# Optimization experiments

Measured on AMD Instinct MI355X. Metric: run time of the kernel, lower is better.

Reference implementation:

```python
import math
import jax, jax.numpy as jnp
import numpy as np

V, D, H, F, L = 32128, 768, 12, 3072, 12
NUM_BUCKETS, MAX_DIST = 32, 128
B, S = 16, 512
EPS = 1e-6


def _rel_bucket(rel_pos, num_buckets=NUM_BUCKETS, max_distance=MAX_DIST):
    # bidirectional T5 bucketing
    num_buckets //= 2
    ret = (rel_pos > 0).astype(jnp.int32) * num_buckets
    n = jnp.abs(rel_pos)
    max_exact = num_buckets // 2
    is_small = n < max_exact
    large = max_exact + (
        jnp.log(n.astype(jnp.float32) / max_exact)
        / math.log(max_distance / max_exact)
        * (num_buckets - max_exact)
    ).astype(jnp.int32)
    large = jnp.minimum(large, num_buckets - 1)
    return ret + jnp.where(is_small, n.astype(jnp.int32), large)


def t5_layernorm(x, w):
    # RMS norm: no mean subtraction, no bias
    var = jnp.mean(x * x, axis=-1, keepdims=True)
    return x * jax.lax.rsqrt(var + EPS) * w


def setup_inputs() -> dict:
    key = jax.random.key(0)
    ks = jax.random.split(key, 12)
    sc = 0.02
    inp = {
        "tokens": jax.random.randint(ks[0], (B, S), 0, V, dtype=jnp.int64),
        "emb": jax.random.normal(ks[1], (V, D), jnp.float32) * sc,
        "rel_bias": jax.random.normal(ks[2], (NUM_BUCKETS, H), jnp.float32) * sc,
        "ln1_w": jnp.ones((L, D), jnp.float32),
        "wq": jax.random.normal(ks[3], (L, D, D), jnp.float32) * sc,
        "wk": jax.random.normal(ks[4], (L, D, D), jnp.float32) * sc,
        "wv": jax.random.normal(ks[5], (L, D, D), jnp.float32) * sc,
        "wo": jax.random.normal(ks[6], (L, D, D), jnp.float32) * sc,
        "ln2_w": jnp.ones((L, D), jnp.float32),
        "w1": jax.random.normal(ks[7], (L, D, F), jnp.float32) * sc,
        "w2": jax.random.normal(ks[8], (L, F, D), jnp.float32) * sc,
        "ln_final_w": jnp.ones((D,), jnp.float32),
    }
    return inp


def _attn(x, pos_bias, wq, wk, wv, wo):
    b, s, d = x.shape
    dh = d // H
    q = (x @ wq).reshape(b, s, H, dh).transpose(0, 2, 1, 3)
    k = (x @ wk).reshape(b, s, H, dh).transpose(0, 2, 1, 3)
    v = (x @ wv).reshape(b, s, H, dh).transpose(0, 2, 1, 3)
    # T5: NO 1/sqrt(dh) scaling; add bucketed relative-position bias
    scores = jnp.einsum("bhqd,bhkd->bhqk", q, k) + pos_bias[None]  # [B,H,S,S]
    a = jax.nn.softmax(scores, axis=-1)
    o = jnp.einsum("bhqk,bhkd->bhqd", a, v)
    o = o.transpose(0, 2, 1, 3).reshape(b, s, d)
    return o @ wo


def reference(tokens, emb, rel_bias, ln1_w, wq, wk, wv, wo, ln2_w, w1, w2, ln_final_w):
    x = emb[tokens]  # [B,S,D]
    s = tokens.shape[1]
    pos = jnp.arange(s)
    buckets = _rel_bucket(pos[None, :] - pos[:, None])  # [S,S]
    pos_bias = rel_bias[buckets].transpose(2, 0, 1)  # [H,S,S], computed once (layer 0)
    for i in range(L):
        h = t5_layernorm(x, ln1_w[i])
        x = x + _attn(h, pos_bias, wq[i], wk[i], wv[i], wo[i])
        h = t5_layernorm(x, ln2_w[i])
        x = x + jax.nn.relu(h @ w1[i]) @ w2[i]
    return t5_layernorm(x, ln_final_w)
```

## Files before the change

### kernel.cpp

```cpp
#include <hip/hip_runtime.h>
#include <hip/hip_bf16.h>

typedef unsigned short u16;
typedef unsigned int   u32;
typedef __attribute__((ext_vector_type(8))) __bf16 bf16x8;
typedef __attribute__((ext_vector_type(4))) float  f32x4;
typedef __attribute__((ext_vector_type(4))) u16    u16x4;
typedef __attribute__((ext_vector_type(4))) u32    u32x4;

#define SEQ     512
#define DMODEL  768
#define NHEAD   12
#define DHEAD   64
#define FDIM    3072
#define NLAYER  12
#define NROWS   8192
#define QKVN    2304

__device__ __forceinline__ u16 f2bf(float f) {
  union { float f; u32 u; } x; x.f = f;
  u32 r = x.u + 0x7fffu + ((x.u >> 16) & 1u);
  return (u16)(r >> 16);
}
__device__ __forceinline__ float u2f(u32 u) { union { u32 u; float f; } x; x.u = u; return x.f; }

__global__ __launch_bounds__(256) void k_transpose_cvt(const float* __restrict__ in,
                                                       u16* __restrict__ out, int K, int N,
                                                       size_t istride, size_t ostride) {
  __shared__ float tile[32][33];
  in  += (size_t)blockIdx.z * istride;
  out += (size_t)blockIdx.z * ostride;
  int nb = blockIdx.x * 32, kb = blockIdx.y * 32;
  int tx = threadIdx.x, ty = threadIdx.y;
#pragma unroll
  for (int i = 0; i < 4; i++)
    tile[ty + 8 * i][tx] = in[(size_t)(kb + ty + 8 * i) * N + nb + tx];
  __syncthreads();
#pragma unroll
  for (int i = 0; i < 4; i++)
    out[(size_t)(nb + ty + 8 * i) * K + kb + tx] = f2bf(tile[tx][ty + 8 * i]);
}

__global__ __launch_bounds__(256) void k_embed(const int* __restrict__ tokens,
                                               const float* __restrict__ emb,
                                               float* __restrict__ x) {
  int idx = blockIdx.x * 256 + threadIdx.x;
  int row = idx / 192, c4 = idx % 192;
  int tok = tokens[row];
  reinterpret_cast<float4*>(x + (size_t)row * DMODEL)[c4] =
      reinterpret_cast<const float4*>(emb + (size_t)tok * DMODEL)[c4];
}

__global__ __launch_bounds__(256) void k_biaslut(const float* __restrict__ rel_bias,
                                                 float* __restrict__ lut) {
  int idx = blockIdx.x * 256 + threadIdx.x;
  int h = idx >> 10, i = idx & 1023;
  int rel = i - 511;
  int ret = rel > 0 ? 16 : 0;
  int n = rel < 0 ? -rel : rel;
  int b;
  if (n < 8) {
    b = n;
  } else {
    float r = logf((float)n * 0.125f) / 2.772588722239781f * 8.0f;
    int lg = 8 + (int)r;
    b = lg < 15 ? lg : 15;
  }
  b += ret;
  lut[idx] = rel_bias[b * NHEAD + h];
}

template <int BF16OUT>
__global__ __launch_bounds__(256) void k_rmsnorm(const float* __restrict__ x,
                                                 const float* __restrict__ w,
                                                 void* __restrict__ out) {
  int row = blockIdx.x * 4 + (threadIdx.x >> 6);
  int lane = threadIdx.x & 63;
  const float4* xr = reinterpret_cast<const float4*>(x + (size_t)row * DMODEL);
  float4 a = xr[lane], b = xr[lane + 64], c = xr[lane + 128];
  float ss = a.x * a.x + a.y * a.y + a.z * a.z + a.w * a.w
           + b.x * b.x + b.y * b.y + b.z * b.z + b.w * b.w
           + c.x * c.x + c.y * c.y + c.z * c.z + c.w * c.w;
#pragma unroll
  for (int off = 1; off < 64; off <<= 1) ss += __shfl_xor(ss, off);
  float sc = rsqrtf(ss * (1.0f / 768.0f) + 1e-6f);
  const float4* wr = reinterpret_cast<const float4*>(w);
  float4 w0 = wr[lane], w1 = wr[lane + 64], w2 = wr[lane + 128];
  if (BF16OUT) {
    u16x4* o = reinterpret_cast<u16x4*>((u16*)out + (size_t)row * DMODEL);
    u16x4 v0, v1, v2;
    v0[0] = f2bf(a.x * sc * w0.x); v0[1] = f2bf(a.y * sc * w0.y);
    v0[2] = f2bf(a.z * sc * w0.z); v0[3] = f2bf(a.w * sc * w0.w);
    v1[0] = f2bf(b.x * sc * w1.x); v1[1] = f2bf(b.y * sc * w1.y);
    v1[2] = f2bf(b.z * sc * w1.z); v1[3] = f2bf(b.w * sc * w1.w);
    v2[0] = f2bf(c.x * sc * w2.x); v2[1] = f2bf(c.y * sc * w2.y);
    v2[2] = f2bf(c.z * sc * w2.z); v2[3] = f2bf(c.w * sc * w2.w);
    o[lane] = v0; o[lane + 64] = v1; o[lane + 128] = v2;
  } else {
    float4* o = reinterpret_cast<float4*>((float*)out + (size_t)row * DMODEL);
    float4 v0, v1, v2;
    v0.x = a.x * sc * w0.x; v0.y = a.y * sc * w0.y; v0.z = a.z * sc * w0.z; v0.w = a.w * sc * w0.w;
    v1.x = b.x * sc * w1.x; v1.y = b.y * sc * w1.y; v1.z = b.z * sc * w1.z; v1.w = b.w * sc * w1.w;
    v2.x = c.x * sc * w2.x; v2.y = c.y * sc * w2.y; v2.z = c.z * sc * w2.z; v2.w = c.w * sc * w2.w;
    o[lane] = v0; o[lane + 64] = v1; o[lane + 128] = v2;
  }
}

__device__ __forceinline__ void gload_lds16(const void* g, void* l) {
  __builtin_amdgcn_global_load_lds((const __attribute__((address_space(1))) void*)g,
                                   (__attribute__((address_space(3))) void*)l, 16, 0, 0);
}

template <int EPI>
__global__ __launch_bounds__(512, 2) void k_gemm(const u16* __restrict__ A, const u16* __restrict__ Bt,
                                                 u16* __restrict__ outb, float* __restrict__ outf,
                                                 int M, int N, int K) {
  __shared__ u16 lds[3 * 24576];
  const int NT = K >> 6;
  int tid = threadIdx.x;
  int lane = tid & 63, wid = tid >> 6;
  int lr = lane & 15, lh = lane >> 4;
  int wm = wid >> 1, wn = wid & 1;

  int gx = gridDim.x;
  int gm = gridDim.y;
  int nwg = gx * gm;
  int linear = blockIdx.y * gx + blockIdx.x;
  int cpx = nwg >> 3;
  int swz = (linear & 7) * cpx + (linear >> 3);
  int bm = (swz % gm) * 256;
  int bn = (swz / gm) * 128;

  const u16* Ab = A  + (size_t)bm * K;
  const u16* Bb = Bt + (size_t)bn * K;

  int cswz = (((tid & 3) ^ ((tid >> 2) & 3) ^ ((tid >> 4) & 3))) * 8;
  int arow = tid >> 2;

  f32x4 acc[4][4] = {};

  auto STAGE_A = [&](int kt, u16* dst) {
#pragma unroll
    for (int a = 0; a < 4; a++) {
      const u16* src = Ab + (size_t)((a & 1) * 128 + arow) * K + kt * 64 + (a >> 1) * 32 + cswz;
      gload_lds16(src, dst + a * 4096 + (size_t)tid * 8);
    }
  };
  auto STAGE_B = [&](int kt, u16* dst) {
#pragma unroll
    for (int b = 0; b < 2; b++) {
      const u16* src = Bb + (size_t)arow * K + kt * 64 + b * 32 + cswz;
      gload_lds16(src, dst + 16384 + b * 4096 + (size_t)tid * 8);
    }
  };

  STAGE_A(0, lds);
  STAGE_B(0, lds);
  STAGE_A(1, lds + 24576);
  STAGE_B(1, lds + 24576);
  asm volatile("s_waitcnt vmcnt(6)" ::: "memory");
  __builtin_amdgcn_s_barrier();

  bf16x8 af[4], bfr[4];
  int rsw = ((lr & 3) ^ ((lr >> 2) & 3)) * 8;
  int chunk = (lh * 8) ^ rsw;

#define DSA(KK)                                                                 \
  _Pragma("unroll") for (int i = 0; i < 4; i++) {                               \
    int row = wm * 64 + i * 16 + lr;                                            \
    af[i] = *reinterpret_cast<const bf16x8*>(cur + (KK) * 8192 + row * 32 + chunk); \
  }
#define DSB(KK)                                                                 \
  _Pragma("unroll") for (int n = 0; n < 4; n++) {                               \
    int row = wn * 64 + n * 16 + lr;                                            \
    bfr[n] = *reinterpret_cast<const bf16x8*>(cur + 16384 + (KK) * 4096 + row * 32 + chunk); \
  }
#define MFMA16                                                                  \
  __builtin_amdgcn_s_setprio(1);                                                \
  _Pragma("unroll") for (int i = 0; i < 4; i++)                                 \
  _Pragma("unroll") for (int n = 0; n < 4; n++)                                 \
    acc[i][n] = __builtin_amdgcn_mfma_f32_16x16x32_bf16(af[i], bfr[n], acc[i][n], 0, 0, 0); \
  __builtin_amdgcn_s_setprio(0);
#define BAR_LGKM                                                                \
  __builtin_amdgcn_s_barrier();                                                 \
  asm volatile("s_waitcnt lgkmcnt(0)" ::: "memory");                            \
  __builtin_amdgcn_sched_barrier(0);

  int cur_s = 0;
  for (int t = 0; t < NT; ++t) {
    const u16* cur = lds + cur_s * 24576;
    int dst_s = cur_s + 2; if (dst_s >= 3) dst_s -= 3;
    u16* dst = lds + dst_s * 24576;
    int t2 = (t + 2 < NT) ? t + 2 : t + 2 - NT;

    DSA(0)
    DSB(0)
    STAGE_A(t2, dst);
    BAR_LGKM
    MFMA16
    __builtin_amdgcn_s_barrier();

    DSA(1)
    DSB(1)
    STAGE_B(t2, dst);
    BAR_LGKM
    MFMA16
    asm volatile("s_waitcnt vmcnt(6)" ::: "memory");
    __builtin_amdgcn_s_barrier();

    cur_s += 1; if (cur_s >= 3) cur_s -= 3;
  }
#undef DSA
#undef DSB
#undef MFMA16
#undef BAR_LGKM

#pragma unroll
  for (int i = 0; i < 4; i++)
#pragma unroll
    for (int n = 0; n < 4; n++)
#pragma unroll
      for (int r = 0; r < 4; r++) {
        int row = bm + wm * 64 + i * 16 + lh * 4 + r;
        int col = bn + wn * 64 + n * 16 + lr;
        size_t idx = (size_t)row * N + col;
        float v = acc[i][n][r];
        if (EPI == 0)      outb[idx] = f2bf(v);
        else if (EPI == 1) outb[idx] = f2bf(v > 0.f ? v : 0.f);
        else               outf[idx] += v;
      }
}

__global__ __launch_bounds__(256) void k_vtrans(const u16* __restrict__ qkv, u16* __restrict__ vt) {
  __shared__ u16 t[32][33];
  int bh = blockIdx.z;
  int b = bh / NHEAD, h = bh % NHEAD;
  int d0 = blockIdx.x * 32, s0 = blockIdx.y * 32;
  int tx = threadIdx.x, ty = threadIdx.y;
  const u16* src = qkv + (size_t)(b * SEQ + s0) * QKVN + 2 * DMODEL + h * DHEAD + d0;
#pragma unroll
  for (int i = 0; i < 4; i++)
    t[ty + 8 * i][tx] = src[(size_t)(ty + 8 * i) * QKVN + tx];
  __syncthreads();
  u16* dst = vt + ((size_t)bh * DHEAD + d0) * SEQ + s0;
#pragma unroll
  for (int i = 0; i < 4; i++)
    dst[(size_t)(ty + 8 * i) * SEQ + tx] = t[tx][ty + 8 * i];
}

__global__ __launch_bounds__(256) void k_attn(const u16* __restrict__ qkv,
                                              const u16* __restrict__ vt,
                                              const float* __restrict__ lutg,
                                              u16* __restrict__ ob) {
  __shared__ __align__(16) float lut[1024];
  __shared__ __align__(16) u16 Ks[2][4096];
  __shared__ __align__(16) u16 Vs[2][4096];
  __shared__ __align__(16) u16 Ps[4][2048];
  int b = blockIdx.x / NHEAD, h = blockIdx.x % NHEAD;
  int qt = blockIdx.y;
  int tid = threadIdx.x;
  int lane = tid & 63, wid = tid >> 6;
  int lr = lane & 15, lh = lane >> 4;
  int q0 = qt * 128 + wid * 32;

  reinterpret_cast<float4*>(lut)[tid] = reinterpret_cast<const float4*>(lutg + h * 1024)[tid];

  bf16x8 aq[2][2];
#pragma unroll
  for (int m = 0; m < 2; m++) {
    const u16* qp = qkv + (size_t)(b * SEQ + q0 + m * 16 + lr) * QKVN + h * DHEAD;
#pragma unroll
    for (int kk = 0; kk < 2; kk++)
      aq[m][kk] = *reinterpret_cast<const bf16x8*>(qp + kk * 32 + lh * 8);
  }

  float mrun[2][4], lpart[2][4];
  f32x4 acc_o[2][4] = {};
#pragma unroll
  for (int m = 0; m < 2; m++)
#pragma unroll
    for (int r = 0; r < 4; r++) { mrun[m][r] = -3.0e38f; lpart[m][r] = 0.f; }

  int srow = tid >> 3, sc8 = tid & 7;
  int scs = (sc8 ^ (srow & 7)) << 3;
  const u16* kbase = qkv + (size_t)(b * SEQ + srow) * QKVN + DMODEL + h * DHEAD + scs;
  const u16* vbase = vt + ((size_t)blockIdx.x * DHEAD + srow) * SEQ + scs;

  auto STAGE = [&](int kt, int bufi) {
    int kv0 = kt << 6;
    gload_lds16(kbase + (size_t)kv0 * QKVN,        &Ks[bufi][tid * 8]);
    gload_lds16(kbase + (size_t)(kv0 + 32) * QKVN, &Ks[bufi][2048 + tid * 8]);
    gload_lds16(vbase + kv0,                       &Vs[bufi][tid * 8]);
    gload_lds16(vbase + 32 * SEQ + kv0,            &Vs[bufi][2048 + tid * 8]);
  };

  STAGE(0, 0);
  asm volatile("s_waitcnt vmcnt(0) lgkmcnt(0)" ::: "memory");
  __builtin_amdgcn_s_barrier();

  int ibase = 511 + lr - q0 - lh * 4;
  u16* pw = Ps[wid];

  for (int kt = 0; kt < 8; kt++) {
    int cb = kt & 1;
    __builtin_amdgcn_s_barrier();
    STAGE((kt + 1) & 7, cb ^ 1);
    asm volatile("s_waitcnt vmcnt(4)" ::: "memory");
    __builtin_amdgcn_s_barrier();

    const u16* KsC = Ks[cb];
    const u16* VsC = Vs[cb];
    int kv0 = kt << 6;

    f32x4 sc[2][4] = {};
#pragma unroll
    for (int kk = 0; kk < 2; kk++) {
      bf16x8 bk[4];
#pragma unroll
      for (int n = 0; n < 4; n++) {
        int row = n * 16 + lr;
        int c = (kk * 4 + lh) ^ (lr & 7);
        bk[n] = *reinterpret_cast<const bf16x8*>(KsC + row * 64 + c * 8);
      }
#pragma unroll
      for (int m = 0; m < 2; m++)
#pragma unroll
        for (int n = 0; n < 4; n++)
          sc[m][n] = __builtin_amdgcn_mfma_f32_16x16x32_bf16(aq[m][kk], bk[n], sc[m][n], 0, 0, 0);
    }

    int pred = 1;
    float vmax[2][4];
#pragma unroll
    for (int m = 0; m < 2; m++)
#pragma unroll
      for (int r = 0; r < 4; r++) {
        int ib = ibase + kv0 - m * 16 - r;
#pragma unroll
        for (int n = 0; n < 4; n++)
          sc[m][n][r] += lut[ib + n * 16];
        float v = fmaxf(fmaxf(sc[m][0][r], sc[m][1][r]), fmaxf(sc[m][2][r], sc[m][3][r]));
        v = fmaxf(v, __shfl_xor(v, 1));
        v = fmaxf(v, __shfl_xor(v, 2));
        v = fmaxf(v, __shfl_xor(v, 4));
        v = fmaxf(v, __shfl_xor(v, 8));
        vmax[m][r] = v;
        pred = pred && (v <= mrun[m][r] + 8.0f);
      }
    if (!__all(pred)) {
#pragma unroll
      for (int m = 0; m < 2; m++)
#pragma unroll
        for (int r = 0; r < 4; r++) {
          float mo = mrun[m][r];
          float mn = fmaxf(mo, vmax[m][r]);
          float corr = __expf(mo - mn);
          mrun[m][r] = mn;
          lpart[m][r] *= corr;
#pragma unroll
          for (int n = 0; n < 4; n++) acc_o[m][n][r] *= corr;
        }
    }
#pragma unroll
    for (int m = 0; m < 2; m++)
#pragma unroll
      for (int r = 0; r < 4; r++) {
        float mm = mrun[m][r];
        int prow = m * 16 + lh * 4 + r;
        int pbse = prow * 64;
        int sw = prow & 7;
        float lp = lpart[m][r];
#pragma unroll
        for (int n = 0; n < 4; n++) {
          float pv = __expf(sc[m][n][r] - mm);
          lp += pv;
          pw[pbse + ((((n << 1) | (lr >> 3)) ^ sw) << 3) + (lr & 7)] = f2bf(pv);
        }
        lpart[m][r] = lp;
      }

    asm volatile("s_waitcnt lgkmcnt(0)" ::: "memory");
    __builtin_amdgcn_sched_barrier(0);
#pragma unroll
    for (int kk = 0; kk < 2; kk++) {
      bf16x8 bvv[4], ap[2];
#pragma unroll
      for (int n = 0; n < 4; n++) {
        int row = n * 16 + lr;
        int c = (kk * 4 + lh) ^ (lr & 7);
        bvv[n] = *reinterpret_cast<const bf16x8*>(VsC + row * 64 + c * 8);
      }
#pragma unroll
      for (int m = 0; m < 2; m++) {
        int row = m * 16 + lr;
        int c = (kk * 4 + lh) ^ (lr & 7);
        ap[m] = *reinterpret_cast<const bf16x8*>(pw + row * 64 + c * 8);
      }
#pragma unroll
      for (int m = 0; m < 2; m++)
#pragma unroll
        for (int n = 0; n < 4; n++)
          acc_o[m][n] = __builtin_amdgcn_mfma_f32_16x16x32_bf16(ap[m], bvv[n], acc_o[m][n], 0, 0, 0);
    }
  }

#pragma unroll
  for (int m = 0; m < 2; m++)
#pragma unroll
    for (int r = 0; r < 4; r++) {
      float l = lpart[m][r];
      l += __shfl_xor(l, 1);
      l += __shfl_xor(l, 2);
      l += __shfl_xor(l, 4);
      l += __shfl_xor(l, 8);
      float inv = 1.f / l;
      size_t orow = (size_t)(b * SEQ + q0 + m * 16 + lh * 4 + r);
#pragma unroll
      for (int n = 0; n < 4; n++)
        ob[orow * DMODEL + h * DHEAD + n * 16 + lr] = f2bf(acc_o[m][n][r] * inv);
    }
}

extern "C" void kernel_launch(void* const* d_in, const int* in_sizes, int n_in,
                              void* d_out, int out_size, void* d_ws, size_t ws_size,
                              hipStream_t stream) {
  const int*   tokens = (const int*)  d_in[0];
  const float* emb    = (const float*)d_in[1];
  const float* relb   = (const float*)d_in[2];
  const float* ln1w   = (const float*)d_in[3];
  const float* wq     = (const float*)d_in[4];
  const float* wk     = (const float*)d_in[5];
  const float* wv     = (const float*)d_in[6];
  const float* wo     = (const float*)d_in[7];
  const float* ln2w   = (const float*)d_in[8];
  const float* w1     = (const float*)d_in[9];
  const float* w2     = (const float*)d_in[10];
  const float* lnfw   = (const float*)d_in[11];
  float* out = (float*)d_out;

  char* p = (char*)d_ws;
  auto carve = [&](size_t bytes) { char* r = p; p += (bytes + 255) & ~(size_t)255; return r; };
  const size_t DD = (size_t)DMODEL * DMODEL, DF = (size_t)DMODEL * FDIM;

  u16*   wqkv_t = (u16*)carve(NLAYER * 3 * DD * 2);
  u16*   wo_t   = (u16*)carve(NLAYER * DD * 2);
  u16*   w1_t   = (u16*)carve(NLAYER * DF * 2);
  u16*   w2_t   = (u16*)carve(NLAYER * DF * 2);
  float* x      = (float*)carve((size_t)NROWS * DMODEL * 4);
  u16*   hbuf   = (u16*)carve((size_t)NROWS * DMODEL * 2);
  u16*   qkvbuf = (u16*)carve((size_t)NROWS * QKVN * 2);
  u16*   abuf   = (u16*)carve((size_t)NROWS * DMODEL * 2);
  u16*   fbuf   = (u16*)carve((size_t)NROWS * FDIM * 2);
  float* lutbuf = (float*)carve((size_t)NHEAD * 1024 * 4);
  u16*   vtbuf  = fbuf;

  dim3 tb(32, 8);
  k_transpose_cvt<<<dim3(24, 24, NLAYER), tb, 0, stream>>>(wq, wqkv_t,          DMODEL, DMODEL, DD, 3 * DD);
  k_transpose_cvt<<<dim3(24, 24, NLAYER), tb, 0, stream>>>(wk, wqkv_t + DD,     DMODEL, DMODEL, DD, 3 * DD);
  k_transpose_cvt<<<dim3(24, 24, NLAYER), tb, 0, stream>>>(wv, wqkv_t + 2 * DD, DMODEL, DMODEL, DD, 3 * DD);
  k_transpose_cvt<<<dim3(24, 24, NLAYER), tb, 0, stream>>>(wo, wo_t,            DMODEL, DMODEL, DD, DD);
  k_transpose_cvt<<<dim3(96, 24, NLAYER), tb, 0, stream>>>(w1, w1_t,            DMODEL, FDIM,   DF, DF);
  k_transpose_cvt<<<dim3(24, 96, NLAYER), tb, 0, stream>>>(w2, w2_t,            FDIM, DMODEL,   DF, DF);

  k_embed<<<NROWS * 192 / 256, 256, 0, stream>>>(tokens, emb, x);
  k_biaslut<<<48, 256, 0, stream>>>(relb, lutbuf);

  for (int i = 0; i < NLAYER; i++) {
    k_rmsnorm<1><<<NROWS / 4, 256, 0, stream>>>(x, ln1w + i * DMODEL, hbuf);
    k_gemm<0><<<dim3(18, 32), 512, 0, stream>>>(hbuf, wqkv_t + (size_t)i * 3 * DD, qkvbuf, nullptr, NROWS, QKVN, DMODEL);
    k_vtrans<<<dim3(2, 16, 192), tb, 0, stream>>>(qkvbuf, vtbuf);
    k_attn<<<dim3(192, 4), 256, 0, stream>>>(qkvbuf, vtbuf, lutbuf, abuf);
    k_gemm<2><<<dim3(6, 32),  512, 0, stream>>>(abuf, wo_t + (size_t)i * DD, nullptr, x, NROWS, DMODEL, DMODEL);
    k_rmsnorm<1><<<NROWS / 4, 256, 0, stream>>>(x, ln2w + i * DMODEL, hbuf);
    k_gemm<1><<<dim3(24, 32), 512, 0, stream>>>(hbuf, w1_t + (size_t)i * DF, fbuf, nullptr, NROWS, FDIM, DMODEL);
    k_gemm<2><<<dim3(6, 32),  512, 0, stream>>>(fbuf, w2_t + (size_t)i * DF, nullptr, x, NROWS, DMODEL, FDIM);
  }
  k_rmsnorm<0><<<NROWS / 4, 256, 0, stream>>>(x, lnfw, out);
}
```

Measured before the change: 3.602 ms.

## Retile GEMM to 128x192 blocks with 4 waves and 32-wide K steps

Reworks the GEMM kernel from 256x128 tiles with 8 waves and K-step 64 to 128x192 tiles with 4 waves and K-step 32. Each wave now owns a 128x48 output slice, reuses its B fragments across both M halves, and the LDS footprint per stage shrinks. Grids change so the projection and FFN GEMMs launch more, smaller blocks, which should improve fill for the N=768 GEMMs (4x64=256 blocks instead of 6x32=192). The trade-offs are twice as many barriers per K, fewer waves to hide latency, and lower arithmetic intensity per block.

After: 3.731 ms. 3.6% more time.

```diff
diff --git a/kernel.cpp b/kernel.cpp
--- a/kernel.cpp
+++ b/kernel.cpp
@@ -112,15 +112,14 @@
 }
 
 template <int EPI>
-__global__ __launch_bounds__(512, 2) void k_gemm(const u16* __restrict__ A, const u16* __restrict__ Bt,
+__global__ __launch_bounds__(256, 2) void k_gemm(const u16* __restrict__ A, const u16* __restrict__ Bt,
                                                  u16* __restrict__ outb, float* __restrict__ outf,
                                                  int M, int N, int K) {
-  __shared__ u16 lds[3 * 24576];
-  const int NT = K >> 6;
+  __shared__ u16 lds[3 * 10240];
+  const int NT = K >> 5;
   int tid = threadIdx.x;
   int lane = tid & 63, wid = tid >> 6;
   int lr = lane & 15, lh = lane >> 4;
-  int wm = wid >> 1, wn = wid & 1;
 
   int gx = gridDim.x;
   int gm = gridDim.y;
@@ -128,58 +127,60 @@
   int linear = blockIdx.y * gx + blockIdx.x;
   int cpx = nwg >> 3;
   int swz = (linear & 7) * cpx + (linear >> 3);
-  int bm = (swz % gm) * 256;
-  int bn = (swz / gm) * 128;
+  int bm = (swz % gm) * 128;
+  int bn = (swz / gm) * 192;
 
   const u16* Ab = A  + (size_t)bm * K;
   const u16* Bb = Bt + (size_t)bn * K;
 
-  int cswz = (((tid & 3) ^ ((tid >> 2) & 3) ^ ((tid >> 4) & 3))) * 8;
-  int arow = tid >> 2;
-
-  f32x4 acc[4][4] = {};
+  f32x4 acc[8][3] = {};
 
   auto STAGE_A = [&](int kt, u16* dst) {
 #pragma unroll
-    for (int a = 0; a < 4; a++) {
-      const u16* src = Ab + (size_t)((a & 1) * 128 + arow) * K + kt * 64 + (a >> 1) * 32 + cswz;
-      gload_lds16(src, dst + a * 4096 + (size_t)tid * 8);
+    for (int a = 0; a < 2; a++) {
+      int elem = a * 256 + tid;
+      int row = elem >> 2, ch = elem & 3;
+      int chs = ch ^ (row & 3) ^ ((row >> 2) & 3);
+      gload_lds16(Ab + (size_t)row * K + kt * 32 + chs * 8, dst + elem * 8);
     }
   };
   auto STAGE_B = [&](int kt, u16* dst) {
 #pragma unroll
-    for (int b = 0; b < 2; b++) {
-      const u16* src = Bb + (size_t)arow * K + kt * 64 + b * 32 + cswz;
-      gload_lds16(src, dst + 16384 + b * 4096 + (size_t)tid * 8);
+    for (int b = 0; b < 3; b++) {
+      int elem = b * 256 + tid;
+      int row = elem >> 2, ch = elem & 3;
+      int chs = ch ^ (row & 3) ^ ((row >> 2) & 3);
+      gload_lds16(Bb + (size_t)row * K + kt * 32 + chs * 8, dst + 4096 + elem * 8);
     }
   };
 
   STAGE_A(0, lds);
   STAGE_B(0, lds);
-  STAGE_A(1, lds + 24576);
-  STAGE_B(1, lds + 24576);
-  asm volatile("s_waitcnt vmcnt(6)" ::: "memory");
+  STAGE_A(1, lds + 10240);
+  STAGE_B(1, lds + 10240);
+  asm volatile("s_waitcnt vmcnt(5)" ::: "memory");
   __builtin_amdgcn_s_barrier();
 
-  bf16x8 af[4], bfr[4];
-  int rsw = ((lr & 3) ^ ((lr >> 2) & 3)) * 8;
-  int chunk = (lh * 8) ^ rsw;
-
-#define DSA(KK)                                                                 \
+  bf16x8 af[4], bfr[3];
+  int fsw = (lr & 3) ^ ((lr >> 2) & 3);
+  int chunk = (lh ^ fsw) * 8;
+
+#define DSA(H)                                                                  \
   _Pragma("unroll") for (int i = 0; i < 4; i++) {                               \
-    int row = wm * 64 + i * 16 + lr;                                            \
-    af[i] = *reinterpret_cast<const bf16x8*>(cur + (KK) * 8192 + row * 32 + chunk); \
-  }
-#define DSB(KK)                                                                 \
-  _Pragma("unroll") for (int n = 0; n < 4; n++) {                               \
-    int row = wn * 64 + n * 16 + lr;                                            \
-    bfr[n] = *reinterpret_cast<const bf16x8*>(cur + 16384 + (KK) * 4096 + row * 32 + chunk); \
-  }
-#define MFMA16                                                                  \
+    int row = (H) * 64 + i * 16 + lr;                                           \
+    af[i] = *reinterpret_cast<const bf16x8*>(cur + row * 32 + chunk);           \
+  }
+#define DSB                                                                     \
+  _Pragma("unroll") for (int n = 0; n < 3; n++) {                               \
+    int row = wid * 48 + n * 16 + lr;                                           \
+    bfr[n] = *reinterpret_cast<const bf16x8*>(cur + 4096 + row * 32 + chunk);   \
+  }
+#define MFMA12(H)                                                               \
   __builtin_amdgcn_s_setprio(1);                                                \
   _Pragma("unroll") for (int i = 0; i < 4; i++)                                 \
-  _Pragma("unroll") for (int n = 0; n < 4; n++)                                 \
-    acc[i][n] = __builtin_amdgcn_mfma_f32_16x16x32_bf16(af[i], bfr[n], acc[i][n], 0, 0, 0); \
+  _Pragma("unroll") for (int n = 0; n < 3; n++)                                 \
+    acc[(H) * 4 + i][n] =                                                       \
+        __builtin_amdgcn_mfma_f32_16x16x32_bf16(af[i], bfr[n], acc[(H) * 4 + i][n], 0, 0, 0); \
   __builtin_amdgcn_s_setprio(0);
 #define BAR_LGKM                                                                \
   __builtin_amdgcn_s_barrier();                                                 \
@@ -188,43 +189,42 @@
 
   int cur_s = 0;
   for (int t = 0; t < NT; ++t) {
-    const u16* cur = lds + cur_s * 24576;
+    const u16* cur = lds + cur_s * 10240;
     int dst_s = cur_s + 2; if (dst_s >= 3) dst_s -= 3;
-    u16* dst = lds + dst_s * 24576;
-    int t2 = (t + 2 < NT) ? t + 2 : t + 2 - NT;
-
+    u16* dst = lds + dst_s * 10240;
+    int t2 = t + 2; if (t2 >= NT) t2 -= NT;
+
+    DSB
     DSA(0)
-    DSB(0)
     STAGE_A(t2, dst);
     BAR_LGKM
-    MFMA16
+    MFMA12(0)
     __builtin_amdgcn_s_barrier();
 
     DSA(1)
-    DSB(1)
     STAGE_B(t2, dst);
     BAR_LGKM
-    MFMA16
-    asm volatile("s_waitcnt vmcnt(6)" ::: "memory");
+    MFMA12(1)
+    asm volatile("s_waitcnt vmcnt(5)" ::: "memory");
     __builtin_amdgcn_s_barrier();
 
     cur_s += 1; if (cur_s >= 3) cur_s -= 3;
   }
 #undef DSA
 #undef DSB
-#undef MFMA16
+#undef MFMA12
 #undef BAR_LGKM
 
 #pragma unroll
-  for (int i = 0; i < 4; i++)
-#pragma unroll
-    for (int n = 0; n < 4; n++)
+  for (int mq = 0; mq < 8; mq++)
+#pragma unroll
+    for (int n = 0; n < 3; n++)
 #pragma unroll
       for (int r = 0; r < 4; r++) {
-        int row = bm + wm * 64 + i * 16 + lh * 4 + r;
-        int col = bn + wn * 64 + n * 16 + lr;
+        int row = bm + mq * 16 + lh * 4 + r;
+        int col = bn + wid * 48 + n * 16 + lr;
         size_t idx = (size_t)row * N + col;
-        float v = acc[i][n][r];
+        float v = acc[mq][n][r];
         if (EPI == 0)      outb[idx] = f2bf(v);
         else if (EPI == 1) outb[idx] = f2bf(v > 0.f ? v : 0.f);
         else               outf[idx] += v;
@@ -467,13 +467,13 @@
 
   for (int i = 0; i < NLAYER; i++) {
     k_rmsnorm<1><<<NROWS / 4, 256, 0, stream>>>(x, ln1w + i * DMODEL, hbuf);
-    k_gemm<0><<<dim3(18, 32), 512, 0, stream>>>(hbuf, wqkv_t + (size_t)i * 3 * DD, qkvbuf, nullptr, NROWS, QKVN, DMODEL);
+    k_gemm<0><<<dim3(12, 64), 256, 0, stream>>>(hbuf, wqkv_t + (size_t)i * 3 * DD, qkvbuf, nullptr, NROWS, QKVN, DMODEL);
     k_vtrans<<<dim3(2, 16, 192), tb, 0, stream>>>(qkvbuf, vtbuf);
     k_attn<<<dim3(192, 4), 256, 0, stream>>>(qkvbuf, vtbuf, lutbuf, abuf);
-    k_gemm<2><<<dim3(6, 32),  512, 0, stream>>>(abuf, wo_t + (size_t)i * DD, nullptr, x, NROWS, DMODEL, DMODEL);
+    k_gemm<2><<<dim3(4, 64),  256, 0, stream>>>(abuf, wo_t + (size_t)i * DD, nullptr, x, NROWS, DMODEL, DMODEL);
     k_rmsnorm<1><<<NROWS / 4, 256, 0, stream>>>(x, ln2w + i * DMODEL, hbuf);
-    k_gemm<1><<<dim3(24, 32), 512, 0, stream>>>(hbuf, w1_t + (size_t)i * DF, fbuf, nullptr, NROWS, FDIM, DMODEL);
-    k_gemm<2><<<dim3(6, 32),  512, 0, stream>>>(fbuf, w2_t + (size_t)i * DF, nullptr, x, NROWS, DMODEL, FDIM);
+    k_gemm<1><<<dim3(16, 64), 256, 0, stream>>>(hbuf, w1_t + (size_t)i * DF, fbuf, nullptr, NROWS, FDIM, DMODEL);
+    k_gemm<2><<<dim3(4, 64),  256, 0, stream>>>(fbuf, w2_t + (size_t)i * DF, nullptr, x, NROWS, DMODEL, FDIM);
   }
   k_rmsnorm<0><<<NROWS / 4, 256, 0, stream>>>(x, lnfw, out);
 }
```

## Use 256x256 GEMM tiles with split-K atomics for the residual projections

Applied to the files above, without the earlier changes.

The GEMM kernel moves from a 256x128 tile with a triple-buffered LDS ring to a 256x256 tile. It uses a double-buffered 64KB LDS layout with an XOR-swizzled row layout and 8 waves arranged 2x4, each computing 128x64. The A and B stages are staggered across quarter-steps. The N=768 output projection and FFN-down GEMMs now split K across grid z (2 and 4 ways) and accumulate into the fp32 residual with atomicAdd. This raises arithmetic intensity per tile and restores enough workgroups for the narrow GEMMs. The cost is atomic traffic, a nondeterministic summation order, and higher register pressure from 32 accumulators per lane.

Result: slower. 4.149 ms (+15.2%).

```diff
diff --git a/kernel.cpp b/kernel.cpp
--- a/kernel.cpp
+++ b/kernel.cpp
@@ -6,7 +6,6 @@
 typedef __attribute__((ext_vector_type(8))) __bf16 bf16x8;
 typedef __attribute__((ext_vector_type(4))) float  f32x4;
 typedef __attribute__((ext_vector_type(4))) u16    u16x4;
-typedef __attribute__((ext_vector_type(4))) u32    u32x4;
 
 #define SEQ     512
 #define DMODEL  768
@@ -22,7 +21,6 @@
   u32 r = x.u + 0x7fffu + ((x.u >> 16) & 1u);
   return (u16)(r >> 16);
 }
-__device__ __forceinline__ float u2f(u32 u) { union { u32 u; float f; } x; x.u = u; return x.f; }
 
 __global__ __launch_bounds__(256) void k_transpose_cvt(const float* __restrict__ in,
                                                        u16* __restrict__ out, int K, int N,
@@ -111,123 +109,126 @@
                                    (__attribute__((address_space(3))) void*)l, 16, 0, 0);
 }
 
+__device__ __forceinline__ bf16x8 rdfrag(const u16* base, int r, int kk, int lh) {
+  return *reinterpret_cast<const bf16x8*>(base + r * 64 + (((kk * 4 + lh) ^ (r & 7)) * 8));
+}
+
 template <int EPI>
 __global__ __launch_bounds__(512, 2) void k_gemm(const u16* __restrict__ A, const u16* __restrict__ Bt,
                                                  u16* __restrict__ outb, float* __restrict__ outf,
-                                                 int M, int N, int K) {
-  __shared__ u16 lds[3 * 24576];
-  const int NT = K >> 6;
+                                                 int M, int N, int K, int Ksub) {
+  __shared__ u16 lds[65536];
+  const int NT = Ksub >> 6;
   int tid = threadIdx.x;
   int lane = tid & 63, wid = tid >> 6;
   int lr = lane & 15, lh = lane >> 4;
-  int wm = wid >> 1, wn = wid & 1;
-
-  int gx = gridDim.x;
-  int gm = gridDim.y;
-  int nwg = gx * gm;
-  int linear = blockIdx.y * gx + blockIdx.x;
+  int wm = wid >> 2, wn = wid & 3;
+
+  int gx = gridDim.x, gm = gridDim.y;
+  int nwg = gx * gm * gridDim.z;
+  int linear = (blockIdx.z * gm + blockIdx.y) * gx + blockIdx.x;
   int cpx = nwg >> 3;
   int swz = (linear & 7) * cpx + (linear >> 3);
-  int bm = (swz % gm) * 256;
-  int bn = (swz / gm) * 128;
-
-  const u16* Ab = A  + (size_t)bm * K;
-  const u16* Bb = Bt + (size_t)bn * K;
-
-  int cswz = (((tid & 3) ^ ((tid >> 2) & 3) ^ ((tid >> 4) & 3))) * 8;
-  int arow = tid >> 2;
-
-  f32x4 acc[4][4] = {};
-
-  auto STAGE_A = [&](int kt, u16* dst) {
-#pragma unroll
-    for (int a = 0; a < 4; a++) {
-      const u16* src = Ab + (size_t)((a & 1) * 128 + arow) * K + kt * 64 + (a >> 1) * 32 + cswz;
-      gload_lds16(src, dst + a * 4096 + (size_t)tid * 8);
+  int bmi = swz % gm, rest = swz / gm;
+  int bni = rest % gx, zi = rest / gx;
+  int bm = bmi * 256, bn = bni * 256;
+  const u16* Ab = A  + (size_t)bm * K + zi * Ksub;
+  const u16* Bb = Bt + (size_t)bn * K + zi * Ksub;
+
+  f32x4 acc[8][4] = {};
+
+  auto STAGE = [&](const u16* mat, int half, int kt, int bufi, int regidx) {
+    u16* dst = lds + bufi * 32768 + regidx * 8192;
+#pragma unroll
+    for (int i = 0; i < 2; i++) {
+      int elem = i * 512 + tid;
+      int row = elem >> 3, ch = elem & 7;
+      int chs = ch ^ (row & 7);
+      gload_lds16(mat + (size_t)(half * 128 + row) * K + kt * 64 + chs * 8, dst + elem * 8);
     }
   };
-  auto STAGE_B = [&](int kt, u16* dst) {
-#pragma unroll
-    for (int b = 0; b < 2; b++) {
-      const u16* src = Bb + (size_t)arow * K + kt * 64 + b * 32 + cswz;
-      gload_lds16(src, dst + 16384 + b * 4096 + (size_t)tid * 8);
-    }
-  };
-
-  STAGE_A(0, lds);
-  STAGE_B(0, lds);
-  STAGE_A(1, lds + 24576);
-  STAGE_B(1, lds + 24576);
-  asm volatile("s_waitcnt vmcnt(6)" ::: "memory");
+
+  STAGE(Ab, 0, 0, 0, 0); STAGE(Ab, 1, 0, 0, 1);
+  STAGE(Bb, 0, 0, 0, 2); STAGE(Bb, 1, 0, 0, 3);
+  STAGE(Bb, 0, 1, 1, 2); STAGE(Bb, 1, 1, 1, 3);
+  asm volatile("s_waitcnt vmcnt(4)" ::: "memory");
   __builtin_amdgcn_s_barrier();
 
-  bf16x8 af[4], bfr[4];
-  int rsw = ((lr & 3) ^ ((lr >> 2) & 3)) * 8;
-  int chunk = (lh * 8) ^ rsw;
-
-#define DSA(KK)                                                                 \
-  _Pragma("unroll") for (int i = 0; i < 4; i++) {                               \
-    int row = wm * 64 + i * 16 + lr;                                            \
-    af[i] = *reinterpret_cast<const bf16x8*>(cur + (KK) * 8192 + row * 32 + chunk); \
-  }
-#define DSB(KK)                                                                 \
-  _Pragma("unroll") for (int n = 0; n < 4; n++) {                               \
-    int row = wn * 64 + n * 16 + lr;                                            \
-    bfr[n] = *reinterpret_cast<const bf16x8*>(cur + 16384 + (KK) * 4096 + row * 32 + chunk); \
-  }
-#define MFMA16                                                                  \
+  int bcol = (wn & 1) * 64;
+
+#define LGKM0 asm volatile("s_waitcnt lgkmcnt(0)" ::: "memory"); __builtin_amdgcn_sched_barrier(0)
+#define MFMA_Q(MQ, KK)                                                          \
   __builtin_amdgcn_s_setprio(1);                                                \
   _Pragma("unroll") for (int i = 0; i < 4; i++)                                 \
   _Pragma("unroll") for (int n = 0; n < 4; n++)                                 \
-    acc[i][n] = __builtin_amdgcn_mfma_f32_16x16x32_bf16(af[i], bfr[n], acc[i][n], 0, 0, 0); \
+    acc[(MQ) * 4 + i][n] =                                                      \
+        __builtin_amdgcn_mfma_f32_16x16x32_bf16(af[i], bfr[KK][n], acc[(MQ) * 4 + i][n], 0, 0, 0); \
   __builtin_amdgcn_s_setprio(0);
-#define BAR_LGKM                                                                \
-  __builtin_amdgcn_s_barrier();                                                 \
-  asm volatile("s_waitcnt lgkmcnt(0)" ::: "memory");                            \
-  __builtin_amdgcn_sched_barrier(0);
-
-  int cur_s = 0;
+
   for (int t = 0; t < NT; ++t) {
-    const u16* cur = lds + cur_s * 24576;
-    int dst_s = cur_s + 2; if (dst_s >= 3) dst_s -= 3;
-    u16* dst = lds + dst_s * 24576;
+    const u16* bufc = lds + (t & 1) * 32768;
+    const u16* curA = bufc + wm * 8192;
+    const u16* curB = bufc + 16384 + (wn >> 1) * 8192;
+    int t1 = (t + 1 < NT) ? t + 1 : 0;
     int t2 = (t + 2 < NT) ? t + 2 : t + 2 - NT;
-
-    DSA(0)
-    DSB(0)
-    STAGE_A(t2, dst);
-    BAR_LGKM
-    MFMA16
-    __builtin_amdgcn_s_barrier();
-
-    DSA(1)
-    DSB(1)
-    STAGE_B(t2, dst);
-    BAR_LGKM
-    MFMA16
-    asm volatile("s_waitcnt vmcnt(6)" ::: "memory");
-    __builtin_amdgcn_s_barrier();
-
-    cur_s += 1; if (cur_s >= 3) cur_s -= 3;
-  }
-#undef DSA
-#undef DSB
-#undef MFMA16
-#undef BAR_LGKM
-
-#pragma unroll
-  for (int i = 0; i < 4; i++)
-#pragma unroll
-    for (int n = 0; n < 4; n++)
+    int b1 = (t + 1) & 1, b2 = t & 1;
+    bf16x8 bfr[2][4], af[4];
+
+#pragma unroll
+    for (int n = 0; n < 4; n++) {
+      int c = bcol + n * 16 + lr;
+      bfr[0][n] = rdfrag(curB, c, 0, lh);
+      bfr[1][n] = rdfrag(curB, c, 1, lh);
+    }
+#pragma unroll
+    for (int i = 0; i < 4; i++) af[i] = rdfrag(curA, i * 16 + lr, 0, lh);
+    STAGE(Ab, 0, t1, b1, 0);
+    __builtin_amdgcn_s_barrier();
+    LGKM0;
+    MFMA_Q(0, 0)
+    __builtin_amdgcn_s_barrier();
+
+#pragma unroll
+    for (int i = 0; i < 4; i++) af[i] = rdfrag(curA, i * 16 + lr, 1, lh);
+    STAGE(Ab, 1, t1, b1, 1);
+    __builtin_amdgcn_s_barrier();
+    LGKM0;
+    MFMA_Q(0, 1)
+    __builtin_amdgcn_s_barrier();
+
+#pragma unroll
+    for (int i = 0; i < 4; i++) af[i] = rdfrag(curA, 64 + i * 16 + lr, 0, lh);
+    STAGE(Bb, 0, t2, b2, 2);
+    __builtin_amdgcn_s_barrier();
+    LGKM0;
+    MFMA_Q(1, 0)
+    __builtin_amdgcn_s_barrier();
+
+#pragma unroll
+    for (int i = 0; i < 4; i++) af[i] = rdfrag(curA, 64 + i * 16 + lr, 1, lh);
+    STAGE(Bb, 1, t2, b2, 3);
+    asm volatile("s_waitcnt vmcnt(4)" ::: "memory");
+    __builtin_amdgcn_s_barrier();
+    LGKM0;
+    MFMA_Q(1, 1)
+    __builtin_amdgcn_s_barrier();
+  }
+#undef MFMA_Q
+#undef LGKM0
+
+#pragma unroll
+  for (int mf = 0; mf < 8; mf++)
+#pragma unroll
+    for (int nf = 0; nf < 4; nf++)
 #pragma unroll
       for (int r = 0; r < 4; r++) {
-        int row = bm + wm * 64 + i * 16 + lh * 4 + r;
-        int col = bn + wn * 64 + n * 16 + lr;
+        int row = bm + wm * 128 + mf * 16 + lh * 4 + r;
+        int col = bn + wn * 64 + nf * 16 + lr;
         size_t idx = (size_t)row * N + col;
-        float v = acc[i][n][r];
+        float v = acc[mf][nf][r];
         if (EPI == 0)      outb[idx] = f2bf(v);
         else if (EPI == 1) outb[idx] = f2bf(v > 0.f ? v : 0.f);
-        else               outf[idx] += v;
+        else               atomicAdd(&outf[idx], v);
       }
 }
 
@@ -467,13 +468,17 @@
 
   for (int i = 0; i < NLAYER; i++) {
     k_rmsnorm<1><<<NROWS / 4, 256, 0, stream>>>(x, ln1w + i * DMODEL, hbuf);
-    k_gemm<0><<<dim3(18, 32), 512, 0, stream>>>(hbuf, wqkv_t + (size_t)i * 3 * DD, qkvbuf, nullptr, NROWS, QKVN, DMODEL);
+    k_gemm<0><<<dim3(9, 32, 1), 512, 0, stream>>>(hbuf, wqkv_t + (size_t)i * 3 * DD, qkvbuf, nullptr,
+                                                  NROWS, QKVN, DMODEL, DMODEL);
     k_vtrans<<<dim3(2, 16, 192), tb, 0, stream>>>(qkvbuf, vtbuf);
     k_attn<<<dim3(192, 4), 256, 0, stream>>>(qkvbuf, vtbuf, lutbuf, abuf);
-    k_gemm<2><<<dim3(6, 32),  512, 0, stream>>>(abuf, wo_t + (size_t)i * DD, nullptr, x, NROWS, DMODEL, DMODEL);
+    k_gemm<3><<<dim3(3, 32, 2), 512, 0, stream>>>(abuf, wo_t + (size_t)i * DD, nullptr, x,
+                                                  NROWS, DMODEL, DMODEL, DMODEL / 2);
     k_rmsnorm<1><<<NROWS / 4, 256, 0, stream>>>(x, ln2w + i * DMODEL, hbuf);
-    k_gemm<1><<<dim3(24, 32), 512, 0, stream>>>(hbuf, w1_t + (size_t)i * DF, fbuf, nullptr, NROWS, FDIM, DMODEL);
-    k_gemm<2><<<dim3(6, 32),  512, 0, stream>>>(fbuf, w2_t + (size_t)i * DF, nullptr, x, NROWS, DMODEL, FDIM);
+    k_gemm<1><<<dim3(12, 32, 1), 512, 0, stream>>>(hbuf, w1_t + (size_t)i * DF, fbuf, nullptr,
+                                                   NROWS, FDIM, DMODEL, DMODEL);
+    k_gemm<3><<<dim3(3, 32, 4), 512, 0, stream>>>(fbuf, w2_t + (size_t)i * DF, nullptr, x,
+                                                  NROWS, DMODEL, FDIM, FDIM / 4);
   }
   k_rmsnorm<0><<<NROWS / 4, 256, 0, stream>>>(x, lnfw, out);
 }
```

## Shrink GEMM tile to 128x128 with K=32 stages and 256-thread blocks

Applied to the files above, without the earlier changes.

Replaces the 256x128 tile, 512-thread GEMM with a 128x128 tile, 4-wave block that stages K in 32-wide slices through a smaller triple-buffered LDS ring. The single-phase loop and simpler swizzle cut LDS use per block, so three blocks can share a CU and the grids double in size. The cost is less operand reuse per loaded byte, about twice as many barrier iterations, and more global traffic for the A and B tiles.

Result: slower. 3.745 ms (+4.0%).

```diff
diff --git a/kernel.cpp b/kernel.cpp
--- a/kernel.cpp
+++ b/kernel.cpp
@@ -6,7 +6,6 @@
 typedef __attribute__((ext_vector_type(8))) __bf16 bf16x8;
 typedef __attribute__((ext_vector_type(4))) float  f32x4;
 typedef __attribute__((ext_vector_type(4))) u16    u16x4;
-typedef __attribute__((ext_vector_type(4))) u32    u32x4;
 
 #define SEQ     512
 #define DMODEL  768
@@ -22,7 +21,6 @@
   u32 r = x.u + 0x7fffu + ((x.u >> 16) & 1u);
   return (u16)(r >> 16);
 }
-__device__ __forceinline__ float u2f(u32 u) { union { u32 u; float f; } x; x.u = u; return x.f; }
 
 __global__ __launch_bounds__(256) void k_transpose_cvt(const float* __restrict__ in,
                                                        u16* __restrict__ out, int K, int N,
@@ -112,108 +110,77 @@
 }
 
 template <int EPI>
-__global__ __launch_bounds__(512, 2) void k_gemm(const u16* __restrict__ A, const u16* __restrict__ Bt,
+__global__ __launch_bounds__(256, 3) void k_gemm(const u16* __restrict__ A, const u16* __restrict__ Bt,
                                                  u16* __restrict__ outb, float* __restrict__ outf,
                                                  int M, int N, int K) {
-  __shared__ u16 lds[3 * 24576];
-  const int NT = K >> 6;
+  __shared__ u16 lds[3 * 8192];
+  const int NT = K >> 5;
   int tid = threadIdx.x;
   int lane = tid & 63, wid = tid >> 6;
   int lr = lane & 15, lh = lane >> 4;
   int wm = wid >> 1, wn = wid & 1;
 
-  int gx = gridDim.x;
-  int gm = gridDim.y;
+  int gx = gridDim.x, gm = gridDim.y;
   int nwg = gx * gm;
   int linear = blockIdx.y * gx + blockIdx.x;
   int cpx = nwg >> 3;
   int swz = (linear & 7) * cpx + (linear >> 3);
-  int bm = (swz % gm) * 256;
+  int bm = (swz % gm) * 128;
   int bn = (swz / gm) * 128;
 
   const u16* Ab = A  + (size_t)bm * K;
   const u16* Bb = Bt + (size_t)bn * K;
 
-  int cswz = (((tid & 3) ^ ((tid >> 2) & 3) ^ ((tid >> 4) & 3))) * 8;
-  int arow = tid >> 2;
-
   f32x4 acc[4][4] = {};
 
-  auto STAGE_A = [&](int kt, u16* dst) {
-#pragma unroll
-    for (int a = 0; a < 4; a++) {
-      const u16* src = Ab + (size_t)((a & 1) * 128 + arow) * K + kt * 64 + (a >> 1) * 32 + cswz;
-      gload_lds16(src, dst + a * 4096 + (size_t)tid * 8);
+  auto STAGE = [&](int kt, u16* buf) {
+#pragma unroll
+    for (int i = 0; i < 2; i++) {
+      int elem = i * 256 + tid;
+      int row = elem >> 2, pc = elem & 3;
+      int chs = pc ^ (row & 3);
+      gload_lds16(Ab + (size_t)row * K + kt * 32 + chs * 8, buf + elem * 8);
+      gload_lds16(Bb + (size_t)row * K + kt * 32 + chs * 8, buf + 4096 + elem * 8);
     }
   };
-  auto STAGE_B = [&](int kt, u16* dst) {
-#pragma unroll
-    for (int b = 0; b < 2; b++) {
-      const u16* src = Bb + (size_t)arow * K + kt * 64 + b * 32 + cswz;
-      gload_lds16(src, dst + 16384 + b * 4096 + (size_t)tid * 8);
-    }
-  };
-
-  STAGE_A(0, lds);
-  STAGE_B(0, lds);
-  STAGE_A(1, lds + 24576);
-  STAGE_B(1, lds + 24576);
-  asm volatile("s_waitcnt vmcnt(6)" ::: "memory");
+
+  STAGE(0, lds);
+  STAGE(1, lds + 8192);
+  asm volatile("s_waitcnt vmcnt(4)" ::: "memory");
   __builtin_amdgcn_s_barrier();
 
-  bf16x8 af[4], bfr[4];
-  int rsw = ((lr & 3) ^ ((lr >> 2) & 3)) * 8;
-  int chunk = (lh * 8) ^ rsw;
-
-#define DSA(KK)                                                                 \
-  _Pragma("unroll") for (int i = 0; i < 4; i++) {                               \
-    int row = wm * 64 + i * 16 + lr;                                            \
-    af[i] = *reinterpret_cast<const bf16x8*>(cur + (KK) * 8192 + row * 32 + chunk); \
-  }
-#define DSB(KK)                                                                 \
-  _Pragma("unroll") for (int n = 0; n < 4; n++) {                               \
-    int row = wn * 64 + n * 16 + lr;                                            \
-    bfr[n] = *reinterpret_cast<const bf16x8*>(cur + 16384 + (KK) * 4096 + row * 32 + chunk); \
-  }
-#define MFMA16                                                                  \
-  __builtin_amdgcn_s_setprio(1);                                                \
-  _Pragma("unroll") for (int i = 0; i < 4; i++)                                 \
-  _Pragma("unroll") for (int n = 0; n < 4; n++)                                 \
-    acc[i][n] = __builtin_amdgcn_mfma_f32_16x16x32_bf16(af[i], bfr[n], acc[i][n], 0, 0, 0); \
-  __builtin_amdgcn_s_setprio(0);
-#define BAR_LGKM                                                                \
-  __builtin_amdgcn_s_barrier();                                                 \
-  asm volatile("s_waitcnt lgkmcnt(0)" ::: "memory");                            \
-  __builtin_amdgcn_sched_barrier(0);
-
-  int cur_s = 0;
+  int cs = 0;
   for (int t = 0; t < NT; ++t) {
-    const u16* cur = lds + cur_s * 24576;
-    int dst_s = cur_s + 2; if (dst_s >= 3) dst_s -= 3;
-    u16* dst = lds + dst_s * 24576;
-    int t2 = (t + 2 < NT) ? t + 2 : t + 2 - NT;
-
-    DSA(0)
-    DSB(0)
-    STAGE_A(t2, dst);
-    BAR_LGKM
-    MFMA16
+    const u16* cur = lds + cs * 8192;
+    int ds = cs + 2; if (ds >= 3) ds -= 3;
+    int t2 = t + 2; if (t2 >= NT) t2 -= NT;
+
+    bf16x8 af[4], bfr[4];
+#pragma unroll
+    for (int i = 0; i < 4; i++) {
+      int r = wm * 64 + i * 16 + lr;
+      af[i] = *reinterpret_cast<const bf16x8*>(cur + r * 32 + ((lh ^ (r & 3)) * 8));
+    }
+#pragma unroll
+    for (int n = 0; n < 4; n++) {
+      int r = wn * 64 + n * 16 + lr;
+      bfr[n] = *reinterpret_cast<const bf16x8*>(cur + 4096 + r * 32 + ((lh ^ (r & 3)) * 8));
+    }
+    STAGE(t2, lds + ds * 8192);
     __builtin_amdgcn_s_barrier();
-
-    DSA(1)
-    DSB(1)
-    STAGE_B(t2, dst);
-    BAR_LGKM
-    MFMA16
-    asm volatile("s_waitcnt vmcnt(6)" ::: "memory");
+    asm volatile("s_waitcnt lgkmcnt(0)" ::: "memory");
+    __builtin_amdgcn_sched_barrier(0);
+    __builtin_amdgcn_s_setprio(1);
+#pragma unroll
+    for (int i = 0; i < 4; i++)
+#pragma unroll
+      for (int n = 0; n < 4; n++)
+        acc[i][n] = __builtin_amdgcn_mfma_f32_16x16x32_bf16(af[i], bfr[n], acc[i][n], 0, 0, 0);
+    __builtin_amdgcn_s_setprio(0);
+    asm volatile("s_waitcnt vmcnt(4)" ::: "memory");
     __builtin_amdgcn_s_barrier();
-
-    cur_s += 1; if (cur_s >= 3) cur_s -= 3;
-  }
-#undef DSA
-#undef DSB
-#undef MFMA16
-#undef BAR_LGKM
+    cs += 1; if (cs >= 3) cs -= 3;
+  }
 
 #pragma unroll
   for (int i = 0; i < 4; i++)
@@ -467,13 +434,17 @@
 
   for (int i = 0; i < NLAYER; i++) {
     k_rmsnorm<1><<<NROWS / 4, 256, 0, stream>>>(x, ln1w + i * DMODEL, hbuf);
-    k_gemm<0><<<dim3(18, 32), 512, 0, stream>>>(hbuf, wqkv_t + (size_t)i * 3 * DD, qkvbuf, nullptr, NROWS, QKVN, DMODEL);
+    k_gemm<0><<<dim3(18, 64), 256, 0, stream>>>(hbuf, wqkv_t + (size_t)i * 3 * DD, qkvbuf, nullptr,
+                                                NROWS, QKVN, DMODEL);
     k_vtrans<<<dim3(2, 16, 192), tb, 0, stream>>>(qkvbuf, vtbuf);
     k_attn<<<dim3(192, 4), 256, 0, stream>>>(qkvbuf, vtbuf, lutbuf, abuf);
-    k_gemm<2><<<dim3(6, 32),  512, 0, stream>>>(abuf, wo_t + (size_t)i * DD, nullptr, x, NROWS, DMODEL, DMODEL);
+    k_gemm<2><<<dim3(6, 64),  256, 0, stream>>>(abuf, wo_t + (size_t)i * DD, nullptr, x,
+                                                NROWS, DMODEL, DMODEL);
     k_rmsnorm<1><<<NROWS / 4, 256, 0, stream>>>(x, ln2w + i * DMODEL, hbuf);
-    k_gemm<1><<<dim3(24, 32), 512, 0, stream>>>(hbuf, w1_t + (size_t)i * DF, fbuf, nullptr, NROWS, FDIM, DMODEL);
-    k_gemm<2><<<dim3(6, 32),  512, 0, stream>>>(fbuf, w2_t + (size_t)i * DF, nullptr, x, NROWS, DMODEL, FDIM);
+    k_gemm<1><<<dim3(24, 64), 256, 0, stream>>>(hbuf, w1_t + (size_t)i * DF, fbuf, nullptr,
+                                                NROWS, FDIM, DMODEL);
+    k_gemm<2><<<dim3(6, 64),  256, 0, stream>>>(fbuf, w2_t + (size_t)i * DF, nullptr, x,
+                                                NROWS, DMODEL, FDIM);
   }
   k_rmsnorm<0><<<NROWS / 4, 256, 0, stream>>>(x, lnfw, out);
 }
```
